# Kernel tuning notes

Measured on AMD Instinct MI355X. Metric: run time of the kernel, lower is better.

Reference implementation:

```python
import jax, jax.numpy as jnp
import numpy as np

N, D = 8192, 256

def setup_inputs() -> dict:
    key = jax.random.key(0)
    k1, k2 = jax.random.split(key)
    data = jnp.zeros((1,), dtype=jnp.float32)  # unused by the module
    Z = jax.random.normal(k1, (N, D), dtype=jnp.float32)
    A_hat = jax.random.uniform(k2, (N, N), dtype=jnp.float32)
    return {"data": data, "Z": Z, "A_hat": A_hat}

def reference(data, Z, A_hat):
    A = A_hat.astype(jnp.float32)
    # D^{-1/2} A D^{-1/2}: diagonal matmuls are mathematically row/col scaling
    d_inv_sqrt = 1.0 / jnp.sqrt(A.sum(axis=1) + 1e-10)  # [N]
    A_norm = A * d_inv_sqrt[:, None] * d_inv_sqrt[None, :]  # [N, N]
    # cosine similarity (F.normalize uses eps=1e-12 clamp on the norm)
    z_norm = jnp.linalg.norm(Z, axis=1, keepdims=True)
    Z_n = Z / jnp.maximum(z_norm, 1e-12)
    similarity = Z_n @ Z_n.T  # [N, N]
    homo_loss = -jnp.sum(A_norm * similarity)
    hetero_loss = jnp.sum((1.0 - A_norm) * similarity)
    return (homo_loss, hetero_loss)
```

## Files before the change

kernel.cpp:

```cpp
#include <hip/hip_runtime.h>
#include <hip/hip_fp16.h>

typedef _Float16 f16x8 __attribute__((ext_vector_type(8)));
typedef _Float16 f16x4 __attribute__((ext_vector_type(4)));
typedef float    f32x4 __attribute__((ext_vector_type(4)));

constexpr int Nn = 8192;
constexpr int Dd = 256;

constexpr int BM = 64;
constexpr int KC = 1024;
constexpr int SK = 128;

__global__ __launch_bounds__(256) void k_rowsum(const float* __restrict__ A,
                                                float* __restrict__ dis,
                                                float* __restrict__ rd) {
    const int row  = blockIdx.x * 4 + (threadIdx.x >> 6);
    const int lane = threadIdx.x & 63;
    const float4* rp = reinterpret_cast<const float4*>(A + (size_t)row * Nn);
    float s = 0.f;
    #pragma unroll
    for (int i = 0; i < Nn / 256; ++i) {
        float4 v = rp[i * 64 + lane];
        s += (v.x + v.y) + (v.z + v.w);
    }
    #pragma unroll
    for (int off = 32; off > 0; off >>= 1) s += __shfl_down(s, off, 64);
    if (lane == 0) {
        float rs = s + 1e-10f;
        dis[row] = rsqrtf(rs);
        rd[row]  = sqrtf(rs);
    }
}

__global__ __launch_bounds__(256) void k_makeYt(const float* __restrict__ Z,
                                               const float* __restrict__ dis,
                                               _Float16* __restrict__ Yt,
                                               _Float16* __restrict__ Yr) {
    __shared__ float nrm[64][4];
    __shared__ _Float16 tile[Dd][72];
    const int t = threadIdx.x;
    const int r = t >> 2, q = t & 3;
    const int row = blockIdx.x * 64 + r;
    const float4* zp = reinterpret_cast<const float4*>(Z + (size_t)row * Dd + q * 64);
    float4 v[16];
    float ss = 0.f;
    #pragma unroll
    for (int i = 0; i < 16; ++i) {
        v[i] = zp[i];
        ss += v[i].x*v[i].x + v[i].y*v[i].y + v[i].z*v[i].z + v[i].w*v[i].w;
    }
    nrm[r][q] = ss;
    __syncthreads();
    const float tot   = nrm[r][0] + nrm[r][1] + nrm[r][2] + nrm[r][3];
    const float scale = dis[row] / fmaxf(sqrtf(tot), 1e-12f);
    #pragma unroll
    for (int i = 0; i < 16; ++i) {
        const int c0 = q * 64 + i * 4;
        f16x4 y = { (_Float16)(v[i].x * scale), (_Float16)(v[i].y * scale),
                    (_Float16)(v[i].z * scale), (_Float16)(v[i].w * scale) };
        tile[c0+0][r] = y[0];
        tile[c0+1][r] = y[1];
        tile[c0+2][r] = y[2];
        tile[c0+3][r] = y[3];
        *reinterpret_cast<f16x4*>(Yr + (size_t)row * Dd + c0) = y;
    }
    __syncthreads();
    int4*       dst = reinterpret_cast<int4*>(Yt + (size_t)t * Nn + blockIdx.x * 64);
    const int4* src = reinterpret_cast<const int4*>(&tile[t][0]);
    #pragma unroll
    for (int i = 0; i < 8; ++i) dst[i] = src[i];
}

__global__ __launch_bounds__(256) void k_colsum(const _Float16* __restrict__ Yt,
                                                const float* __restrict__ rd,
                                                float* __restrict__ s) {
    const int k = blockIdx.x;
    const int t = threadIdx.x;
    const _Float16* yp = Yt + (size_t)k * Nn + t * 32;
    const float*    rp = rd + t * 32;
    float acc = 0.f;
    #pragma unroll
    for (int i = 0; i < 32; ++i) acc += (float)yp[i] * rp[i];
    #pragma unroll
    for (int off = 32; off > 0; off >>= 1) acc += __shfl_down(acc, off, 64);
    __shared__ float red[4];
    if ((t & 63) == 0) red[t >> 6] = acc;
    __syncthreads();
    if (t == 0) s[k] = red[0] + red[1] + red[2] + red[3];
}

__global__ __launch_bounds__(512, 4) void k_main(const float* __restrict__ A,
                                                 const _Float16* __restrict__ Yt,
                                                 const _Float16* __restrict__ Yr,
                                                 float* __restrict__ T) {
    __shared__ _Float16 Ys[Dd * SK];

    const int ib = blockIdx.x & (Nn / BM - 1);
    const int jb = blockIdx.x >> 7;
    const int I0 = ib * BM;
    const int K0 = jb * KC;
    const int w  = threadIdx.x >> 6;
    const int wr = w >> 1;
    const int wn = w & 1;
    const int l  = threadIdx.x & 63;
    const int lr = l & 15;
    const int lk = l >> 4;

    const size_t arow = (size_t)(I0 + wr * 16 + lr) * Nn;

    f32x4 acc[8];
    #pragma unroll
    for (int t = 0; t < 8; ++t) acc[t] = f32x4{0.f, 0.f, 0.f, 0.f};

    #define STAGE(SC)                                                          \
    {   const int kc = K0 + (SC) * SK;                                         \
        _Pragma("unroll")                                                      \
        for (int q = 0; q < 8; ++q) {                                          \
            const int nrow = w * 32 + q * 4 + lk;                              \
            const int sl   = lr ^ (nrow & 15);                                 \
            __builtin_amdgcn_global_load_lds(                                  \
                (const __attribute__((address_space(1))) unsigned int*)        \
                    (Yt + (size_t)nrow * Nn + kc + sl * 8),                    \
                (__attribute__((address_space(3))) unsigned int*)              \
                    (Ys + (w * 32 + q * 4) * SK),                              \
                16, 0, 0);                                                     \
        }                                                                      \
    }

    float4 av[8];
    #define LOADA(SC)                                                          \
    {   const float* ab = A + arow + K0 + (SC) * SK + lk * 8;                  \
        _Pragma("unroll")                                                      \
        for (int ks = 0; ks < 4; ++ks) {                                       \
            av[ks*2+0] = *reinterpret_cast<const float4*>(ab + ks * 32);       \
            av[ks*2+1] = *reinterpret_cast<const float4*>(ab + ks * 32 + 4);   \
        }                                                                      \
    }

    LOADA(0);
    STAGE(0);
    asm volatile("s_waitcnt vmcnt(0)" ::: "memory");
    __syncthreads();

    for (int sc = 0; sc < KC / SK; ++sc) {
        f16x8 af[4];
        #pragma unroll
        for (int ks = 0; ks < 4; ++ks) {
            const float4 a0 = av[ks*2+0], a1 = av[ks*2+1];
            af[ks] = f16x8{ (_Float16)a0.x, (_Float16)a0.y, (_Float16)a0.z, (_Float16)a0.w,
                            (_Float16)a1.x, (_Float16)a1.y, (_Float16)a1.z, (_Float16)a1.w };
        }
        if (sc < KC / SK - 1) LOADA(sc + 1);

        #pragma unroll
        for (int tn = 0; tn < 8; ++tn) {
            const int n = wn * 128 + tn * 16 + lr;
            #pragma unroll
            for (int ks = 0; ks < 4; ++ks) {
                const int sl = (ks * 4 + lk) ^ lr;
                const f16x8 bf = *reinterpret_cast<const f16x8*>(Ys + n * SK + sl * 8);
                acc[tn] = __builtin_amdgcn_mfma_f32_16x16x32_f16(af[ks], bf, acc[tn], 0, 0, 0);
            }
        }
        __syncthreads();
        if (sc < KC / SK - 1) {
            STAGE(sc + 1);
            asm volatile("s_waitcnt vmcnt(0)" ::: "memory");
            __syncthreads();
        }
    }

    float part = 0.f;
    #pragma unroll
    for (int tn = 0; tn < 8; ++tn) {
        const int n = wn * 128 + tn * 16 + lr;
        #pragma unroll
        for (int r = 0; r < 4; ++r) {
            const int i = I0 + wr * 16 + lk * 4 + r;
            part += acc[tn][r] * (float)Yr[(size_t)i * Dd + n];
        }
    }
    #pragma unroll
    for (int off = 32; off > 0; off >>= 1) part += __shfl_down(part, off, 64);
    __shared__ float red[8];
    if (l == 0) red[w] = part;
    __syncthreads();
    if (threadIdx.x == 0) {
        float t = 0.f;
        #pragma unroll
        for (int i = 0; i < 8; ++i) t += red[i];
        atomicAdd(T, t);
    }
}

__global__ __launch_bounds__(256) void k_final(const float* __restrict__ s,
                                               const float* __restrict__ T,
                                               float* __restrict__ out) {
    const int t = threadIdx.x;
    float v = s[t];
    float p = v * v;
    #pragma unroll
    for (int off = 32; off > 0; off >>= 1) p += __shfl_down(p, off, 64);
    __shared__ float red[4];
    if ((t & 63) == 0) red[t >> 6] = p;
    __syncthreads();
    if (t == 0) {
        const float ss = red[0] + red[1] + red[2] + red[3];
        const float Tv = *T;
        out[0] = -Tv;
        out[1] = ss - Tv;
    }
}

extern "C" void kernel_launch(void* const* d_in, const int* in_sizes, int n_in,
                              void* d_out, int out_size, void* d_ws, size_t ws_size,
                              hipStream_t stream) {
    const float* Z = (const float*)d_in[1];
    const float* A = (const float*)d_in[2];
    float* out = (float*)d_out;

    char* ws = (char*)d_ws;
    float*    dis = (float*)(ws);
    float*    rd  = (float*)(ws + 32768);
    float*    s   = (float*)(ws + 65536);
    float*    T   = (float*)(ws + 66560);
    _Float16* Yt  = (_Float16*)(ws + 131072);
    _Float16* Yr  = (_Float16*)(ws + 131072 + (size_t)Nn * Dd * 2);

    hipMemsetAsync(T, 0, sizeof(float), stream);
    k_rowsum<<<Nn / 4, 256, 0, stream>>>(A, dis, rd);
    k_makeYt<<<Nn / 64, 256, 0, stream>>>(Z, dis, Yt, Yr);
    k_colsum<<<Dd, 256, 0, stream>>>(Yt, rd, s);
    k_main<<<(Nn / BM) * (Nn / KC), 512, 0, stream>>>(A, Yt, Yr, T);
    k_final<<<1, 256, 0, stream>>>(s, T, out);
}
```

Measured before the change: 153.1 us.

## Double-buffer Y tile in LDS with halved K-step and drop memset

The main kernel now double-buffers the LDS tile of Yt with half-size K stages. The next stage's global-to-LDS copy and A loads are issued before the MFMA loop on the current buffer, and only a partial vmcnt wait plus one barrier is needed per iteration, replacing the serialised load-wait-compute pattern. The accumulator zeroing moves from a hipMemsetAsync into the rowsum kernel, saving one launch. This doubles the number of loop iterations and changes the LDS swizzle. The partial wait count, which assumes the A loads are ordered relative to the LDS copies, is a correctness risk.

```diff
diff --git a/kernel.cpp b/kernel.cpp
--- a/kernel.cpp
+++ b/kernel.cpp
@@ -10,11 +10,14 @@
 
 constexpr int BM = 64;
 constexpr int KC = 1024;
-constexpr int SK = 128;
+constexpr int SK = 64;
+constexpr int NSC = KC / SK;
 
 __global__ __launch_bounds__(256) void k_rowsum(const float* __restrict__ A,
                                                 float* __restrict__ dis,
-                                                float* __restrict__ rd) {
+                                                float* __restrict__ rd,
+                                                float* __restrict__ T) {
+    if (blockIdx.x == 0 && threadIdx.x == 0) *T = 0.f;
     const int row  = blockIdx.x * 4 + (threadIdx.x >> 6);
     const int lane = threadIdx.x & 63;
     const float4* rp = reinterpret_cast<const float4*>(A + (size_t)row * Nn);
@@ -94,7 +97,7 @@
                                                  const _Float16* __restrict__ Yt,
                                                  const _Float16* __restrict__ Yr,
                                                  float* __restrict__ T) {
-    __shared__ _Float16 Ys[Dd * SK];
+    __shared__ _Float16 Ys[2 * Dd * SK];
 
     const int ib = blockIdx.x & (Nn / BM - 1);
     const int jb = blockIdx.x >> 7;
@@ -113,61 +116,62 @@
     #pragma unroll
     for (int t = 0; t < 8; ++t) acc[t] = f32x4{0.f, 0.f, 0.f, 0.f};
 
-    #define STAGE(SC)                                                          \
+    #define STAGE(SC, BUF)                                                     \
     {   const int kc = K0 + (SC) * SK;                                         \
         _Pragma("unroll")                                                      \
-        for (int q = 0; q < 8; ++q) {                                          \
-            const int nrow = w * 32 + q * 4 + lk;                              \
-            const int sl   = lr ^ (nrow & 15);                                 \
+        for (int q = 0; q < 4; ++q) {                                          \
+            const int nrow = w * 32 + q * 8 + (l >> 3);                        \
+            const int s8   = (l & 7) ^ (l >> 3);                               \
             __builtin_amdgcn_global_load_lds(                                  \
                 (const __attribute__((address_space(1))) unsigned int*)        \
-                    (Yt + (size_t)nrow * Nn + kc + sl * 8),                    \
+                    (Yt + (size_t)nrow * Nn + kc + s8 * 8),                    \
                 (__attribute__((address_space(3))) unsigned int*)              \
-                    (Ys + (w * 32 + q * 4) * SK),                              \
+                    (Ys + (BUF) * (Dd * SK) + (w * 32 + q * 8) * SK),          \
                 16, 0, 0);                                                     \
         }                                                                      \
     }
 
-    float4 av[8];
+    float4 av[4];
     #define LOADA(SC)                                                          \
     {   const float* ab = A + arow + K0 + (SC) * SK + lk * 8;                  \
-        _Pragma("unroll")                                                      \
-        for (int ks = 0; ks < 4; ++ks) {                                       \
-            av[ks*2+0] = *reinterpret_cast<const float4*>(ab + ks * 32);       \
-            av[ks*2+1] = *reinterpret_cast<const float4*>(ab + ks * 32 + 4);   \
-        }                                                                      \
-    }
-
+        av[0] = *reinterpret_cast<const float4*>(ab);                          \
+        av[1] = *reinterpret_cast<const float4*>(ab + 4);                      \
+        av[2] = *reinterpret_cast<const float4*>(ab + 32);                     \
+        av[3] = *reinterpret_cast<const float4*>(ab + 36);                     \
+    }
+
+    STAGE(0, 0);
     LOADA(0);
-    STAGE(0);
     asm volatile("s_waitcnt vmcnt(0)" ::: "memory");
-    __syncthreads();
-
-    for (int sc = 0; sc < KC / SK; ++sc) {
-        f16x8 af[4];
-        #pragma unroll
-        for (int ks = 0; ks < 4; ++ks) {
-            const float4 a0 = av[ks*2+0], a1 = av[ks*2+1];
+    __builtin_amdgcn_s_barrier();
+
+    for (int sc = 0; sc < NSC; ++sc) {
+        const int cur = sc & 1;
+        f16x8 af[2];
+        #pragma unroll
+        for (int ks = 0; ks < 2; ++ks) {
+            const float4 a0 = av[ks*2], a1 = av[ks*2+1];
             af[ks] = f16x8{ (_Float16)a0.x, (_Float16)a0.y, (_Float16)a0.z, (_Float16)a0.w,
                             (_Float16)a1.x, (_Float16)a1.y, (_Float16)a1.z, (_Float16)a1.w };
         }
-        if (sc < KC / SK - 1) LOADA(sc + 1);
-
+        if (sc + 1 < NSC) {
+            STAGE(sc + 1, cur ^ 1);
+            LOADA(sc + 1);
+        }
         #pragma unroll
         for (int tn = 0; tn < 8; ++tn) {
             const int n = wn * 128 + tn * 16 + lr;
             #pragma unroll
-            for (int ks = 0; ks < 4; ++ks) {
-                const int sl = (ks * 4 + lk) ^ lr;
-                const f16x8 bf = *reinterpret_cast<const f16x8*>(Ys + n * SK + sl * 8);
+            for (int ks = 0; ks < 2; ++ks) {
+                const int sl = (ks * 4 + lk) ^ (lr & 7);
+                const f16x8 bf = *reinterpret_cast<const f16x8*>(
+                    Ys + cur * (Dd * SK) + n * SK + sl * 8);
                 acc[tn] = __builtin_amdgcn_mfma_f32_16x16x32_f16(af[ks], bf, acc[tn], 0, 0, 0);
             }
         }
-        __syncthreads();
-        if (sc < KC / SK - 1) {
-            STAGE(sc + 1);
-            asm volatile("s_waitcnt vmcnt(0)" ::: "memory");
-            __syncthreads();
+        if (sc + 1 < NSC) {
+            asm volatile("s_waitcnt vmcnt(4)" ::: "memory");
+            __builtin_amdgcn_s_barrier();
         }
     }
 
@@ -228,8 +232,7 @@
     _Float16* Yt  = (_Float16*)(ws + 131072);
     _Float16* Yr  = (_Float16*)(ws + 131072 + (size_t)Nn * Dd * 2);
 
-    hipMemsetAsync(T, 0, sizeof(float), stream);
-    k_rowsum<<<Nn / 4, 256, 0, stream>>>(A, dis, rd);
+    k_rowsum<<<Nn / 4, 256, 0, stream>>>(A, dis, rd, T);
     k_makeYt<<<Nn / 64, 256, 0, stream>>>(Z, dis, Yt, Yr);
     k_colsum<<<Dd, 256, 0, stream>>>(Yt, rd, s);
     k_main<<<(Nn / BM) * (Nn / KC), 512, 0, stream>>>(A, Yt, Yr, T);
```

Result: no change. 151.1 us (-1.3%).
